# Performance work log

Measured on AMD Instinct MI355X. Metric: run time of the kernel, lower is better.

Reference implementation:

```python
import jax, jax.numpy as jnp
import numpy as np

KSIZE, STRIDE, H, W = 7, 4, 128, 128
NH = (H - KSIZE) // STRIDE + 1  # 31
L = NH * NH                     # 961 patches


def conv2d(x, w, b=None, stride=1):
    y = jax.lax.conv_general_dilated(x, w, (stride, stride), 'VALID',
                                     dimension_numbers=('NCHW', 'OIHW', 'NCHW'))
    if b is not None:
        y = y + b[None, :, None, None]
    return y


def refpad(x):
    return jnp.pad(x, ((0, 0), (0, 0), (1, 1), (1, 1)), mode='reflect')


def unfold(x, k, s):
    # torch.nn.Unfold equivalent, returned as (B, C, k, k, L)
    B, C, Hh, Ww = x.shape
    nh = (Hh - k) // s + 1
    nw = (Ww - k) // s + 1
    hi = (jnp.arange(nh) * s)[:, None] + jnp.arange(k)  # (nh, k)
    wi = (jnp.arange(nw) * s)[:, None] + jnp.arange(k)  # (nw, k)
    p = x[:, :, hi]            # (B, C, nh, k, W)
    p = p[:, :, :, :, wi]      # (B, C, nh, k, nw, k)
    p = p.transpose(0, 1, 3, 5, 2, 4).reshape(B, C, k, k, nh * nw)
    return p


def fold(patches, Hh, Ww, k, s):
    # patches: (B, nh, nw, C, k, k); overlap-add like torch.nn.functional.fold
    B, nh, nw, C = patches.shape[0], patches.shape[1], patches.shape[2], patches.shape[3]
    hi = (jnp.arange(nh) * s)[:, None] + jnp.arange(k)  # (nh, k)
    wi = (jnp.arange(nw) * s)[:, None] + jnp.arange(k)  # (nw, k)
    H_idx = hi[:, None, :, None]  # (nh, 1, k, 1)
    W_idx = wi[None, :, None, :]  # (1, nw, 1, k)
    vals = patches.transpose(0, 3, 1, 2, 4, 5)  # (B, C, nh, nw, k, k)
    out = jnp.zeros((B, C, Hh, Ww), patches.dtype)
    return out.at[:, :, H_idx, W_idx].add(vals)


def setup_inputs() -> dict:
    key = jax.random.key(0)
    ks = jax.random.split(key, 16)
    Cin, Ci = 32, 16            # in_channels, inter_channels
    F_in = KSIZE * KSIZE * Ci   # 784
    F_out = F_in // 4           # 196
    s = 0.05
    d = {
        'x':       jax.random.normal(ks[0], (8, Cin, H, W), jnp.float32),
        'g_w':     jax.random.normal(ks[1], (Ci, Cin, 3, 3), jnp.float32) * s,
        'g_b':     jax.random.normal(ks[2], (Ci,), jnp.float32) * s,
        'w_w':     jax.random.normal(ks[3], (Ci, Cin, 3, 3), jnp.float32) * s,
        'w_b':     jax.random.normal(ks[4], (Ci,), jnp.float32) * s,
        'theta_w': jax.random.normal(ks[5], (Cin, Ci, 1, 1), jnp.float32) * s,
        'theta_b': jax.random.normal(ks[6], (Cin,), jnp.float32) * s,
        'fc1_w':   jax.random.normal(ks[7], (F_out, F_in), jnp.float32) * s,
        'fc1_b':   jax.random.normal(ks[8], (F_out,), jnp.float32) * s,
        'mconv_w': jax.random.normal(ks[9], (L, L), jnp.float32) * s,
        'mconv_b': jax.random.normal(ks[10], (L,), jnp.float32) * s,
        'mfc_w':   jax.random.normal(ks[11], (L, L), jnp.float32) * s,
        'mfc_b':   jax.random.normal(ks[12], (L,), jnp.float32) * s,
        'c1_w':    jax.random.normal(ks[13], (Cin // 2, Cin, 3, 3), jnp.float32) * s,
        'c2_w':    jax.random.normal(ks[14], (Cin, Cin // 2, 1, 1), jnp.float32) * s,
    }
    return d


def reference(x, g_w, g_b, w_w, w_b, theta_w, theta_b, fc1_w, fc1_b,
              mconv_w, mconv_b, mfc_w, mfc_b, c1_w, c2_w):
    residual = x
    x1 = conv2d(refpad(x), g_w, g_b)        # (B, Ci, H, W)
    x2 = conv2d(refpad(x), w_w, w_b)        # (B, Ci, H, W)
    x3 = conv2d(x1, theta_w, theta_b)       # (B, Cin, H, W)
    B = x.shape[0]
    Cin = x.shape[1]

    p6 = unfold(x1, KSIZE, STRIDE).transpose(0, 4, 1, 2, 3).reshape(B, L, -1)   # (B,L,Ci*49)
    p4 = unfold(x2, KSIZE, STRIDE).transpose(0, 4, 1, 2, 3).reshape(B, L, -1)   # (B,L,Ci*49)
    p62 = unfold(x3, KSIZE, STRIDE).transpose(0, 4, 1, 2, 3).reshape(B, L, -1)  # (B,L,Cin*49)

    wf = p4 @ fc1_w.T + fc1_b   # (B, L, F)
    xf = p6 @ fc1_w.T + fc1_b   # (B, L, F)
    A = jnp.einsum('blf,bmf->blm', wf, xf)  # (B, L, L)

    # Ti1 (Conv1d k=1 over patch dim) + Ti2 (Linear over patch dim, transposed)
    Ti = jnp.einsum('nc,bcm->bnm', mconv_w + mfc_w, A) + (mconv_b + mfc_b)[None, :, None]
    mask = jax.nn.sigmoid(Ti)
    mask_b = (mask != 0.0).astype(A.dtype)

    scale = wf.shape[-1] ** -0.5
    Am = jax.nn.softmax(A * mask * scale, axis=-1) * mask_b  # (B, L, L)

    y = jnp.einsum('blm,bmf->blf', Am, p62)  # (B, L, Cin*49)
    y = y.reshape(B, NH, NH, Cin, KSIZE, KSIZE)
    out = fold(y, H, W, KSIZE, STRIDE)       # (B, Cin, H, W)

    # BasicBlock: conv3x3(reflect) -> lrelu -> conv1x1 -> lrelu
    o = jax.nn.leaky_relu(conv2d(refpad(out), c1_w), 0.2)
    o = jax.nn.leaky_relu(conv2d(o, c2_w), 0.2)
    out = residual + o
    return Am, out
```

## Files before the change

### kernel.cpp

```cpp
#include <hip/hip_runtime.h>
#include <math.h>

namespace {
constexpr int Bn   = 8;
constexpr int CIN  = 32;
constexpr int CI   = 16;
constexpr int Lp   = 961;
constexpr int FIN  = 784;
constexpr int FOUT = 196;
constexpr int F62  = 1568;

constexpr int FCP  = 224;
constexpr long long FCB = 961LL * FCP;
constexpr int KP   = 992;
constexpr long long WFTB = 196LL * KP;
constexpr long long AMBB = 961LL * KP;
constexpr long long PBTB = 1568LL * KP;
constexpr long long AB   = 961LL * 961;
constexpr int YLD  = 964;
constexpr long long YB = 1568LL * YLD;
constexpr int CKP  = 512;
}

typedef __attribute__((ext_vector_type(8))) short short8x;
typedef __attribute__((ext_vector_type(4))) float floatx4;
typedef __attribute__((ext_vector_type(4))) unsigned short ushort4x;

static __device__ __forceinline__ unsigned short f2bf(float x) {
    unsigned int u = __builtin_bit_cast(unsigned int, x);
    u += 0x7fffu + ((u >> 16) & 1u);
    return (unsigned short)(u >> 16);
}
static __device__ __forceinline__ float bf2f(unsigned short h) {
    return __builtin_bit_cast(float, ((unsigned int)h) << 16);
}

__global__ __launch_bounds__(256)
void prep_k(const float* __restrict__ g_w, const float* __restrict__ w_w,
            const float* __restrict__ c1_w,
            unsigned short* __restrict__ cwh, unsigned short* __restrict__ cwl,
            unsigned short* __restrict__ c1h, unsigned short* __restrict__ c1l,
            const float* __restrict__ mconv_w, const float* __restrict__ mfc_w,
            unsigned short* __restrict__ Mwh, unsigned short* __restrict__ Mwl,
            const float* __restrict__ mconv_b, const float* __restrict__ mfc_b,
            float* __restrict__ Mb,
            const float* __restrict__ fc1w,
            unsigned short* __restrict__ Wh, unsigned short* __restrict__ Wl,
            unsigned short* __restrict__ wfTh, unsigned short* __restrict__ wfTl)
{
    int i = blockIdx.x * 256 + threadIdx.x;
    if (i < 16384) {
        int n = i >> 9, k = i & 511;
        int ci = k >> 4, t = k & 15;
        float v = 0.0f;
        if (t < 9) v = (n < 16) ? g_w[n * 288 + ci * 9 + t]
                                : w_w[(n - 16) * 288 + ci * 9 + t];
        unsigned short h = f2bf(v);
        cwh[i] = h; cwl[i] = f2bf(v - bf2f(h));
    } else if (i < 24576) {
        int k2 = i - 16384;
        int n = k2 >> 9, k = k2 & 511;
        int ci = k >> 4, t = k & 15;
        float v = (t < 9) ? c1_w[n * 288 + ci * 9 + t] : 0.0f;
        unsigned short h = f2bf(v);
        c1h[k2] = h; c1l[k2] = f2bf(v - bf2f(h));
    } else if (i < 977888) {
        int k = i - 24576;
        int n = k / KP, c = k - n * KP;
        float v = (c < 961) ? (mconv_w[n * 961 + c] + mfc_w[n * 961 + c]) : 0.0f;
        unsigned short h = f2bf(v);
        Mwh[k] = h; Mwl[k] = f2bf(v - bf2f(h));
    } else if (i < 978849) {
        int k = i - 977888;
        Mb[k] = mconv_b[k] + mfc_b[k];
    } else if (i < 1183649) {
        int k = i - 978849;
        int n = k / 800, kk = k - n * 800;
        float v = (n < 196 && kk < 784) ? fc1w[n * 784 + kk] : 0.0f;
        unsigned short h = f2bf(v);
        Wh[k] = h; Wl[k] = f2bf(v - bf2f(h));
    } else if (i < 1233825) {
        int k = i - 1183649;
        int row = k >> 5, c = k & 31;
        long long pos = (long long)row * KP + 960 + c;
        wfTh[pos] = 0; wfTl[pos] = 0;
    }
}

template<int NOUT, bool BIAS, bool LEAKY>
__global__ __launch_bounds__(256)
void convmfma_k(const float* __restrict__ x,
                const unsigned short* __restrict__ Bh,
                const unsigned short* __restrict__ Bl,
                const float* __restrict__ b1, const float* __restrict__ b2,
                float* __restrict__ o1, float* __restrict__ o2)
{
    __shared__ unsigned short AsH[128 * 32], AsL[128 * 32];
    __shared__ unsigned short BsH[NOUT * 32], BsL[NOUT * 32];

    const int tid = threadIdx.x;
    const int b   = blockIdx.x & 7;
    const int h   = blockIdx.x >> 3;
    const float* xb = x + (size_t)b * CIN * 16384;

    const int m   = tid & 127;
    const int kh2 = tid >> 7;
    int ghr[3], gwc[3];
    #pragma unroll
    for (int r = 0; r < 3; ++r) {
        int gh = h - 1 + r; ghr[r] = (gh < 0) ? 1 : (gh > 127 ? 126 : gh);
        int gw = m - 1 + r; gwc[r] = (gw < 0) ? 1 : (gw > 127 ? 126 : gw);
    }

    const int lane = tid & 63;
    const int wv   = tid >> 6;
    const int wm   = wv * 32;
    const int fr   = lane & 15;
    const int kq   = lane >> 4;
    constexpr int NF = NOUT / 16;

    floatx4 acc[2][NF];
    #pragma unroll
    for (int i = 0; i < 2; ++i)
        #pragma unroll
        for (int j = 0; j < NF; ++j)
            acc[i][j] = (floatx4){0.f, 0.f, 0.f, 0.f};

    float pv[9];
    short8x pbh0, pbh1, pbl0, pbl1;
    const bool bstage = tid < NOUT * 2;
    const int bn  = tid >> 1;
    const int bk  = tid & 1;

    auto loadA = [&](int ks) {
        const float* src = xb + (ks * 2 + kh2) * 16384;
        #pragma unroll
        for (int j = 0; j < 9; ++j)
            pv[j] = src[ghr[j / 3] * 128 + gwc[j % 3]];
    };
    auto loadB = [&](int ks) {
        if (bstage) {
            const unsigned short* sh = Bh + bn * CKP + ks * 32 + bk * 16;
            const unsigned short* sl = Bl + bn * CKP + ks * 32 + bk * 16;
            pbh0 = *(const short8x*)sh;       pbh1 = *(const short8x*)(sh + 8);
            pbl0 = *(const short8x*)sl;       pbl1 = *(const short8x*)(sl + 8);
        }
    };

    loadA(0); loadB(0);
    for (int ks = 0; ks < 16; ++ks) {
        {
            unsigned short hv[16], lv[16];
            #pragma unroll
            for (int j = 0; j < 16; ++j) {
                float v = (j < 9) ? pv[j] : 0.0f;
                unsigned short hh = f2bf(v);
                hv[j] = hh; lv[j] = f2bf(v - bf2f(hh));
            }
            const int swz = (m >> 1) & 3;
            const int o0 = (kh2 * 2) ^ swz, o1o = (kh2 * 2 + 1) ^ swz;
            *(short8x*)&AsH[m * 32 + o0 * 8]  = ((short8x*)hv)[0];
            *(short8x*)&AsH[m * 32 + o1o * 8] = ((short8x*)hv)[1];
            *(short8x*)&AsL[m * 32 + o0 * 8]  = ((short8x*)lv)[0];
            *(short8x*)&AsL[m * 32 + o1o * 8] = ((short8x*)lv)[1];
        }
        if (bstage) {
            const int swz = (bn >> 1) & 3;
            const int o0 = (bk * 2) ^ swz, o1o = (bk * 2 + 1) ^ swz;
            *(short8x*)&BsH[bn * 32 + o0 * 8]  = pbh0;
            *(short8x*)&BsH[bn * 32 + o1o * 8] = pbh1;
            *(short8x*)&BsL[bn * 32 + o0 * 8]  = pbl0;
            *(short8x*)&BsL[bn * 32 + o1o * 8] = pbl1;
        }
        __syncthreads();
        if (ks < 15) { loadA(ks + 1); loadB(ks + 1); }

        short8x bhf[NF], blf[NF];
        #pragma unroll
        for (int j = 0; j < NF; ++j) {
            int nr = j * 16 + fr;
            int off = nr * 32 + ((kq ^ ((nr >> 1) & 3)) * 8);
            bhf[j] = *(const short8x*)&BsH[off];
            blf[j] = *(const short8x*)&BsL[off];
        }
        #pragma unroll
        for (int i = 0; i < 2; ++i) {
            int mr = wm + i * 16 + fr;
            int off = mr * 32 + ((kq ^ ((mr >> 1) & 3)) * 8);
            short8x ah = *(const short8x*)&AsH[off];
            short8x al = *(const short8x*)&AsL[off];
            #pragma unroll
            for (int j = 0; j < NF; ++j) {
                acc[i][j] = __builtin_amdgcn_mfma_f32_16x16x32_bf16(ah, bhf[j], acc[i][j], 0, 0, 0);
                acc[i][j] = __builtin_amdgcn_mfma_f32_16x16x32_bf16(ah, blf[j], acc[i][j], 0, 0, 0);
                acc[i][j] = __builtin_amdgcn_mfma_f32_16x16x32_bf16(al, bhf[j], acc[i][j], 0, 0, 0);
            }
        }
        __syncthreads();
    }

    #pragma unroll
    for (int j = 0; j < NF; ++j) {
        int n = j * 16 + fr;
        float bnv = 0.0f;
        if constexpr (BIAS) bnv = (n < 16) ? b1[n] : b2[n - 16];
        float* dst;
        if constexpr (NOUT == 32) {
            dst = (n < 16) ? (o1 + (((size_t)b * 16 + n) * 128 + h) * 128)
                           : (o2 + (((size_t)b * 16 + (n - 16)) * 128 + h) * 128);
        } else {
            dst = o1 + (((size_t)b * 16 + n) * 128 + h) * 128;
        }
        #pragma unroll
        for (int i = 0; i < 2; ++i) {
            int wb = wm + i * 16 + kq * 4;
            floatx4 ov;
            #pragma unroll
            for (int r = 0; r < 4; ++r) {
                float v = acc[i][j][r] + bnv;
                if constexpr (LEAKY) v = (v >= 0.0f) ? v : 0.2f * v;
                ov[r] = v;
            }
            *(floatx4*)(dst + wb) = ov;
        }
    }
}

template<bool BIAS, bool LEAKY, bool RESID>
__global__ __launch_bounds__(256)
void conv1x1p_k(const float* __restrict__ src, const float* __restrict__ wgt,
                const float* __restrict__ bias, const float* __restrict__ resid,
                float* __restrict__ out)
{
    int idx = blockIdx.x * 256 + threadIdx.x;
    int pix = idx & 16383;
    int b   = idx >> 14;
    const float* sb = src + (size_t)b * CI * 16384 + pix;
    float s[16];
    #pragma unroll
    for (int ci = 0; ci < CI; ++ci) s[ci] = sb[ci * 16384];
    size_t ob = (size_t)b * 32 * 16384 + pix;
    #pragma unroll
    for (int co = 0; co < 32; ++co) {
        const float* wrow = wgt + co * CI;
        float acc = BIAS ? bias[co] : 0.0f;
        #pragma unroll
        for (int ci = 0; ci < CI; ++ci) acc += wrow[ci] * s[ci];
        if constexpr (LEAKY) acc = (acc >= 0.0f) ? acc : 0.2f * acc;
        if constexpr (RESID) acc += resid[ob + (size_t)co * 16384];
        out[ob + (size_t)co * 16384] = acc;
    }
}

template<bool WRT>
__global__ __launch_bounds__(256)
void fcmfma_k(const float* __restrict__ xsrc,
              const unsigned short* __restrict__ Wh,
              const unsigned short* __restrict__ Wl,
              const float* __restrict__ bias,
              unsigned short* __restrict__ Dh, unsigned short* __restrict__ Dl,
              unsigned short* __restrict__ DTh, unsigned short* __restrict__ DTl)
{
    __shared__ unsigned short AsH[64*32], AsL[64*32], BsH[64*32], BsL[64*32];
    const int tid = threadIdx.x;
    const int tm0 = (blockIdx.x >> 2) * 64;
    const int tn0 = (blockIdx.x & 3) * 64;

    const int lr = tid >> 2;
    const int lc = tid & 3;
    const int gm = tm0 + lr;
    const bool mok = gm < 7688;
    int gbase = 0;
    if (mok) {
        int b = gm / 961, pi = gm - b * 961;
        int ih = pi / 31, iw = pi - ih * 31;
        gbase = b * 262144 + ih * 512 + iw * 4;
    }
    const int pc = ((lc ^ ((lr >> 1) & 3))) * 8;
    const unsigned short* Whr = Wh + (tn0 + lr) * 800;
    const unsigned short* Wlr = Wl + (tn0 + lr) * 800;

    const int lane = tid & 63, wv = tid >> 6;
    const int wm = (wv >> 1) * 32, wn = (wv & 1) * 32;
    const int fr = lane & 15, kq = lane >> 4;

    floatx4 acc[2][2];
    #pragma unroll
    for (int i = 0; i < 2; ++i)
        #pragma unroll
        for (int j = 0; j < 2; ++j)
            acc[i][j] = (floatx4){0.f, 0.f, 0.f, 0.f};

    float pv[8];
    short8x pwh, pwl;
    auto loadA = [&](int k0) {
        #pragma unroll
        for (int j = 0; j < 8; ++j) {
            int k = k0 + lc * 8 + j;
            float v = 0.0f;
            if (mok && k < 784) {
                int c  = k / 49, r = k - c * 49;
                int kh = r / 7,  kw = r - kh * 7;
                v = xsrc[gbase + c * 16384 + kh * 128 + kw];
            }
            pv[j] = v;
        }
    };
    auto loadW = [&](int k0) {
        pwh = *(const short8x*)(Whr + k0 + lc * 8);
        pwl = *(const short8x*)(Wlr + k0 + lc * 8);
    };

    loadA(0); loadW(0);
    for (int k0 = 0; k0 < 800; k0 += 32) {
        unsigned short hv[8], lv[8];
        #pragma unroll
        for (int j = 0; j < 8; ++j) {
            unsigned short h = f2bf(pv[j]);
            hv[j] = h; lv[j] = f2bf(pv[j] - bf2f(h));
        }
        *(short8x*)&AsH[lr * 32 + pc] = *(short8x*)hv;
        *(short8x*)&AsL[lr * 32 + pc] = *(short8x*)lv;
        *(short8x*)&BsH[lr * 32 + pc] = pwh;
        *(short8x*)&BsL[lr * 32 + pc] = pwl;
        __syncthreads();
        if (k0 + 32 < 800) { loadA(k0 + 32); loadW(k0 + 32); }
        short8x ah[2], al[2], bh[2], bl[2];
        #pragma unroll
        for (int i = 0; i < 2; ++i) {
            int mr = wm + i * 16 + fr;
            int off = mr * 32 + ((kq ^ ((mr >> 1) & 3)) * 8);
            ah[i] = *(const short8x*)&AsH[off];
            al[i] = *(const short8x*)&AsL[off];
        }
        #pragma unroll
        for (int j = 0; j < 2; ++j) {
            int nr = wn + j * 16 + fr;
            int off = nr * 32 + ((kq ^ ((nr >> 1) & 3)) * 8);
            bh[j] = *(const short8x*)&BsH[off];
            bl[j] = *(const short8x*)&BsL[off];
        }
        #pragma unroll
        for (int i = 0; i < 2; ++i)
            #pragma unroll
            for (int j = 0; j < 2; ++j) {
                acc[i][j] = __builtin_amdgcn_mfma_f32_16x16x32_bf16(ah[i], bh[j], acc[i][j], 0, 0, 0);
                acc[i][j] = __builtin_amdgcn_mfma_f32_16x16x32_bf16(ah[i], bl[j], acc[i][j], 0, 0, 0);
                acc[i][j] = __builtin_amdgcn_mfma_f32_16x16x32_bf16(al[i], bh[j], acc[i][j], 0, 0, 0);
            }
        __syncthreads();
    }

    #pragma unroll
    for (int j = 0; j < 2; ++j) {
        int n = tn0 + wn + j * 16 + fr;
        if (n >= FCP) continue;
        float bn = (n < 196) ? bias[n] : 0.0f;
        #pragma unroll
        for (int i = 0; i < 2; ++i) {
            #pragma unroll
            for (int r = 0; r < 4; ++r) {
                int l = tm0 + wm + i * 16 + kq * 4 + r;
                if (l >= 7688) continue;
                int b = l / 961, pi = l - b * 961;
                float v = (n < 196) ? (acc[i][j][r] + bn) : 0.0f;
                unsigned short h = f2bf(v);
                unsigned short lo = f2bf(v - bf2f(h));
                long long base = (long long)b * FCB + (long long)pi * FCP + n;
                Dh[base] = h;
                Dl[base] = lo;
                if constexpr (WRT) {
                    if (n < 196) {
                        long long tb = (long long)b * WFTB + (long long)n * KP + pi;
                        DTh[tb] = h;
                        DTl[tb] = lo;
                    }
                }
            }
        }
    }
}

__global__ __launch_bounds__(256)
void w2mfma_k(const unsigned short* __restrict__ Xhi,
              const unsigned short* __restrict__ Xlo,
              const unsigned short* __restrict__ Yhi,
              const unsigned short* __restrict__ Ylo,
              unsigned short* __restrict__ W2h,
              unsigned short* __restrict__ W2l)
{
    __shared__ unsigned short XsH[4096], XsL[4096], YsH[4096], YsL[4096];
    const int b   = blockIdx.x & 7;
    const int t   = blockIdx.x >> 3;
    const int tm0 = (t >> 1) * 128;
    const int tn0 = (t & 1) * 128;
    const unsigned short* Ybh = Yhi + (long long)b * WFTB;
    const unsigned short* Ybl = Ylo + (long long)b * WFTB;
    const int tid = threadIdx.x;

    const int sr  = tid >> 1;
    const int sc0 = (tid & 1) * 2;
    const bool xok = (tm0 + sr) < 961;
    const bool yok = (tn0 + sr) < 196;
    const unsigned short* Xrh = Xhi + (long long)(tm0 + sr) * KP;
    const unsigned short* Xrl = Xlo + (long long)(tm0 + sr) * KP;
    const unsigned short* Yrh = Ybh + (long long)(tn0 + sr) * KP;
    const unsigned short* Yrl = Ybl + (long long)(tn0 + sr) * KP;
    const int swz = (sr >> 1) & 3;

    const int lane = tid & 63;
    const int wv   = tid >> 6;
    const int wm   = (wv >> 1) * 64, wn = (wv & 1) * 64;
    const int fr   = lane & 15;
    const int kq   = lane >> 4;

    floatx4 acc[4][4];
    #pragma unroll
    for (int i = 0; i < 4; ++i)
        #pragma unroll
        for (int j = 0; j < 4; ++j)
            acc[i][j] = (floatx4){0.f, 0.f, 0.f, 0.f};

    const short8x zz = {0,0,0,0,0,0,0,0};
    short8x pxh[2], pxl[2], pyh[2], pyl[2];
    auto loadK = [&](int k0) {
        #pragma unroll
        for (int c = 0; c < 2; ++c) {
            int kc = sc0 + c;
            pxh[c] = xok ? *(const short8x*)(Xrh + k0 + kc * 8) : zz;
            pxl[c] = xok ? *(const short8x*)(Xrl + k0 + kc * 8) : zz;
            pyh[c] = yok ? *(const short8x*)(Yrh + k0 + kc * 8) : zz;
            pyl[c] = yok ? *(const short8x*)(Yrl + k0 + kc * 8) : zz;
        }
    };

    loadK(0);
    for (int k0 = 0; k0 < KP; k0 += 32) {
        #pragma unroll
        for (int c = 0; c < 2; ++c) {
            int pc = (sc0 + c) ^ swz;
            *(short8x*)&XsH[sr * 32 + pc * 8] = pxh[c];
            *(short8x*)&XsL[sr * 32 + pc * 8] = pxl[c];
            *(short8x*)&YsH[sr * 32 + pc * 8] = pyh[c];
            *(short8x*)&YsL[sr * 32 + pc * 8] = pyl[c];
        }
        __syncthreads();
        if (k0 + 32 < KP) loadK(k0 + 32);
        short8x bh[4], bl[4];
        #pragma unroll
        for (int j = 0; j < 4; ++j) {
            int nr = wn + j * 16 + fr;
            int off = nr * 32 + ((kq ^ ((nr >> 1) & 3)) * 8);
            bh[j] = *(const short8x*)&YsH[off];
            bl[j] = *(const short8x*)&YsL[off];
        }
        #pragma unroll
        for (int i = 0; i < 4; ++i) {
            int mr = wm + i * 16 + fr;
            int off = mr * 32 + ((kq ^ ((mr >> 1) & 3)) * 8);
            short8x ah = *(const short8x*)&XsH[off];
            short8x al = *(const short8x*)&XsL[off];
            #pragma unroll
            for (int j = 0; j < 4; ++j) {
                acc[i][j] = __builtin_amdgcn_mfma_f32_16x16x32_bf16(ah, bh[j], acc[i][j], 0, 0, 0);
                acc[i][j] = __builtin_amdgcn_mfma_f32_16x16x32_bf16(ah, bl[j], acc[i][j], 0, 0, 0);
                acc[i][j] = __builtin_amdgcn_mfma_f32_16x16x32_bf16(al, bh[j], acc[i][j], 0, 0, 0);
            }
        }
        __syncthreads();
    }

    unsigned short* Wh2 = W2h + (long long)b * FCB;
    unsigned short* Wl2 = W2l + (long long)b * FCB;
    #pragma unroll
    for (int j = 0; j < 4; ++j) {
        int f = tn0 + wn + j * 16 + fr;
        if (f >= FCP) continue;
        #pragma unroll
        for (int i = 0; i < 4; ++i) {
            int lb = tm0 + wm + i * 16 + kq * 4;
            #pragma unroll
            for (int r = 0; r < 4; ++r) {
                int l = lb + r;
                if (l >= 961) continue;
                float v = acc[i][j][r];
                unsigned short h = f2bf(v);
                long long pos = (long long)l * FCP + f;
                Wh2[pos] = h;
                Wl2[pos] = f2bf(v - bf2f(h));
            }
        }
    }
}

__global__ __launch_bounds__(256, 2)
void atimfma_k(const unsigned short* __restrict__ Wfh,
               const unsigned short* __restrict__ Wfl,
               const unsigned short* __restrict__ W2h,
               const unsigned short* __restrict__ W2l,
               const unsigned short* __restrict__ Xfh,
               const unsigned short* __restrict__ Xfl,
               const float* __restrict__ Mb,
               float* __restrict__ Sout)
{
    const int b   = blockIdx.x & 7;
    const int t   = blockIdx.x >> 3;
    const int tm0 = (t >> 3) * 128;
    const int tn0 = (t & 7) * 128;
    const int tid = threadIdx.x;

    const int lane = tid & 63;
    const int wv   = tid >> 6;
    const int wm   = (wv >> 1) * 64, wn = (wv & 1) * 64;
    const int fr   = lane & 15;
    const int kq   = lane >> 4;

    const long long bb = (long long)b * FCB;
    const unsigned short* A1h = Wfh + bb;
    const unsigned short* A1l = Wfl + bb;
    const unsigned short* A2h = W2h + bb;
    const unsigned short* A2l = W2l + bb;
    const unsigned short* Byh = Xfh + bb;
    const unsigned short* Byl = Xfl + bb;

    int aoff[4], boff[4];
    #pragma unroll
    for (int i = 0; i < 4; ++i) {
        int r = tm0 + wm + i * 16 + fr; if (r > 960) r = 960;
        aoff[i] = r * FCP + kq * 8;
    }
    #pragma unroll
    for (int j = 0; j < 4; ++j) {
        int r = tn0 + wn + j * 16 + fr; if (r > 960) r = 960;
        boff[j] = r * FCP + kq * 8;
    }

    floatx4 accA[4][4], accT[4][4];
    #pragma unroll
    for (int i = 0; i < 4; ++i)
        #pragma unroll
        for (int j = 0; j < 4; ++j) {
            accA[i][j] = (floatx4){0.f, 0.f, 0.f, 0.f};
            accT[i][j] = (floatx4){0.f, 0.f, 0.f, 0.f};
        }

    short8x f1h[2][4], f1l[2][4], f2h[2][4], f2l[2][4], fbh[2][4], fbl[2][4];

    #pragma unroll
    for (int j = 0; j < 4; ++j) {
        fbh[0][j] = *(const short8x*)(Byh + boff[j]);
        fbl[0][j] = *(const short8x*)(Byl + boff[j]);
    }
    #pragma unroll
    for (int i = 0; i < 4; ++i) {
        f1h[0][i] = *(const short8x*)(A1h + aoff[i]);
        f1l[0][i] = *(const short8x*)(A1l + aoff[i]);
        f2h[0][i] = *(const short8x*)(A2h + aoff[i]);
        f2l[0][i] = *(const short8x*)(A2l + aoff[i]);
    }

    #pragma unroll
    for (int ks = 0; ks < 7; ++ks) {
        const int cur = ks & 1, nxt = cur ^ 1;
        if (ks < 6) {
            const int k0 = (ks + 1) * 32;
            #pragma unroll
            for (int j = 0; j < 4; ++j) {
                fbh[nxt][j] = *(const short8x*)(Byh + boff[j] + k0);
                fbl[nxt][j] = *(const short8x*)(Byl + boff[j] + k0);
            }
            #pragma unroll
            for (int i = 0; i < 4; ++i) {
                f1h[nxt][i] = *(const short8x*)(A1h + aoff[i] + k0);
                f1l[nxt][i] = *(const short8x*)(A1l + aoff[i] + k0);
                f2h[nxt][i] = *(const short8x*)(A2h + aoff[i] + k0);
                f2l[nxt][i] = *(const short8x*)(A2l + aoff[i] + k0);
            }
        }
        #pragma unroll
        for (int i = 0; i < 4; ++i) {
            #pragma unroll
            for (int j = 0; j < 4; ++j) {
                accA[i][j] = __builtin_amdgcn_mfma_f32_16x16x32_bf16(f1h[cur][i], fbh[cur][j], accA[i][j], 0, 0, 0);
                accA[i][j] = __builtin_amdgcn_mfma_f32_16x16x32_bf16(f1h[cur][i], fbl[cur][j], accA[i][j], 0, 0, 0);
                accA[i][j] = __builtin_amdgcn_mfma_f32_16x16x32_bf16(f1l[cur][i], fbh[cur][j], accA[i][j], 0, 0, 0);
                accT[i][j] = __builtin_amdgcn_mfma_f32_16x16x32_bf16(f2h[cur][i], fbh[cur][j], accT[i][j], 0, 0, 0);
                accT[i][j] = __builtin_amdgcn_mfma_f32_16x16x32_bf16(f2h[cur][i], fbl[cur][j], accT[i][j], 0, 0, 0);
                accT[i][j] = __builtin_amdgcn_mfma_f32_16x16x32_bf16(f2l[cur][i], fbh[cur][j], accT[i][j], 0, 0, 0);
            }
        }
    }

    const float scale = 0.07142857142857142f;
    float* Sb = Sout + (long long)b * AB;
    #pragma unroll
    for (int j = 0; j < 4; ++j) {
        int m = tn0 + wn + j * 16 + fr;
        if (m >= 961) continue;
        #pragma unroll
        for (int i = 0; i < 4; ++i) {
            int lb = tm0 + wm + i * 16 + kq * 4;
            #pragma unroll
            for (int r = 0; r < 4; ++r) {
                int l = lb + r;
                if (l >= 961) continue;
                float ti = accT[i][j][r] + Mb[l];
                float mask = 1.0f / (1.0f + expf(-ti));
                Sb[(long long)l * 961 + m] = accA[i][j][r] * mask * scale;
            }
        }
    }
}

__global__ __launch_bounds__(256)
void softmax_mask_k(const float* __restrict__ S, float* __restrict__ Am,
                    unsigned short* __restrict__ Amb)
{
    int row = blockIdx.x;
    const float* srow = S + (long long)row * Lp;
    float*       orow = Am + (long long)row * Lp;
    unsigned short* brow = Amb + (long long)row * KP;
    int tid = threadIdx.x;

    float s[4], mb[4];
    float lmax = -INFINITY;
    #pragma unroll
    for (int j = 0; j < 4; ++j) {
        int m = tid + j * 256;
        if (m < Lp) {
            float v = srow[m];
            s[j]  = v;
            mb[j] = (v != 0.0f) ? 1.0f : 0.0f;
            lmax  = fmaxf(lmax, v);
        } else { s[j] = -INFINITY; mb[j] = 0.0f; }
    }
    __shared__ float red[256];
    red[tid] = lmax; __syncthreads();
    #pragma unroll
    for (int off = 128; off > 0; off >>= 1) {
        if (tid < off) red[tid] = fmaxf(red[tid], red[tid + off]);
        __syncthreads();
    }
    float rmax = red[0];
    __syncthreads();

    float e[4];
    float lsum = 0.0f;
    #pragma unroll
    for (int j = 0; j < 4; ++j) {
        int m = tid + j * 256;
        e[j] = (m < Lp) ? expf(s[j] - rmax) : 0.0f;
        lsum += e[j];
    }
    red[tid] = lsum; __syncthreads();
    #pragma unroll
    for (int off = 128; off > 0; off >>= 1) {
        if (tid < off) red[tid] += red[tid + off];
        __syncthreads();
    }
    float inv = 1.0f / red[0];
    #pragma unroll
    for (int j = 0; j < 4; ++j) {
        int m = tid + j * 256;
        if (m < Lp) {
            float v = e[j] * inv * mb[j];
            orow[m] = v;
            brow[m] = f2bf(v);
        } else if (m < KP) {
            brow[m] = 0;
        }
    }
}

__global__ __launch_bounds__(256)
void p62bt_k(const float* __restrict__ x3, unsigned short* __restrict__ out)
{
    int idx = blockIdx.x * 256 + threadIdx.x;
    if (idx >= 8 * 1568 * 124) return;
    int ck = idx % 124;
    int t  = idx / 124;
    int n  = t % 1568;
    int b  = t / 1568;
    int c = n / 49, rr = n - c * 49;
    int kh = rr / 7, kw = rr - kh * 7;
    const float* src = x3 + (long long)b * 524288 + c * 16384 + kh * 128 + kw;
    int k = ck * 8;
    unsigned short v[8];
    #pragma unroll
    for (int j = 0; j < 8; ++j) {
        int kk = k + j;
        if (kk < Lp) {
            int ih = kk / 31, iw = kk - ih * 31;
            v[j] = f2bf(src[ih * 512 + iw * 4]);
        } else v[j] = 0;
    }
    *(short8x*)(out + ((long long)b * 1568 + n) * KP + k) = *(short8x*)v;
}

__global__ __launch_bounds__(256)
void ymfma_k(const unsigned short* __restrict__ Amb,
             const unsigned short* __restrict__ Pbt,
             unsigned short* __restrict__ yT)
{
    __shared__ unsigned short As[128 * 32];
    __shared__ unsigned short Bs[128 * 32];
    const int b   = blockIdx.x & 7;
    const int t   = blockIdx.x >> 3;
    const int tn0 = (t % 13) * 128;
    const int tm0 = (t / 13) * 128;
    const unsigned short* Ab = Amb + (long long)b * AMBB;
    const unsigned short* Bb = Pbt + (long long)b * PBTB;
    const int tid = threadIdx.x;

    const int sr  = tid >> 1;
    const int sc0 = (tid & 1) * 2;
    const bool aok = (tm0 + sr) < Lp;
    const bool bok = (tn0 + sr) < F62;
    const unsigned short* Arow = Ab + (long long)(tm0 + sr) * KP;
    const unsigned short* Brow = Bb + (long long)(tn0 + sr) * KP;
    const int swz = (sr >> 1) & 3;

    const int lane = tid & 63;
    const int wv   = tid >> 6;
    const int wm   = (wv >> 1) * 64, wn = (wv & 1) * 64;
    const int fr   = lane & 15;
    const int kq   = lane >> 4;

    floatx4 acc[4][4];
    #pragma unroll
    for (int i = 0; i < 4; ++i)
        #pragma unroll
        for (int j = 0; j < 4; ++j)
            acc[i][j] = (floatx4){0.f, 0.f, 0.f, 0.f};

    const short8x zz = {0,0,0,0,0,0,0,0};
    short8x pa[2], pb[2];
    auto loadK = [&](int k0) {
        #pragma unroll
        for (int c = 0; c < 2; ++c) {
            int kc = sc0 + c;
            pa[c] = aok ? *(const short8x*)(Arow + k0 + kc * 8) : zz;
            pb[c] = bok ? *(const short8x*)(Brow + k0 + kc * 8) : zz;
        }
    };

    loadK(0);
    for (int k0 = 0; k0 < Lp; k0 += 32) {
        #pragma unroll
        for (int c = 0; c < 2; ++c) {
            int pc = (sc0 + c) ^ swz;
            *(short8x*)&As[sr * 32 + pc * 8] = pa[c];
            *(short8x*)&Bs[sr * 32 + pc * 8] = pb[c];
        }
        __syncthreads();
        if (k0 + 32 < Lp) loadK(k0 + 32);
        short8x af[4], bfr[4];
        #pragma unroll
        for (int i = 0; i < 4; ++i) {
            int mr = wm + i * 16 + fr;
            af[i] = *(const short8x*)&As[mr * 32 + ((kq ^ ((mr >> 1) & 3)) * 8)];
        }
        #pragma unroll
        for (int j = 0; j < 4; ++j) {
            int nr = wn + j * 16 + fr;
            bfr[j] = *(const short8x*)&Bs[nr * 32 + ((kq ^ ((nr >> 1) & 3)) * 8)];
        }
        #pragma unroll
        for (int i = 0; i < 4; ++i)
            #pragma unroll
            for (int j = 0; j < 4; ++j)
                acc[i][j] = __builtin_amdgcn_mfma_f32_16x16x32_bf16(
                                af[i], bfr[j], acc[i][j], 0, 0, 0);
        __syncthreads();
    }

    unsigned short* Yb = yT + (long long)b * YB;
    #pragma unroll
    for (int j = 0; j < 4; ++j) {
        int n = tn0 + wn + j * 16 + fr;
        if (n >= F62) continue;
        unsigned short* Yr = Yb + (long long)n * YLD;
        #pragma unroll
        for (int i = 0; i < 4; ++i) {
            int lb = tm0 + wm + i * 16 + kq * 4;
            if (lb >= Lp) continue;
            ushort4x hv;
            #pragma unroll
            for (int r = 0; r < 4; ++r) hv[r] = f2bf(acc[i][j][r]);
            if (lb + 3 < Lp) {
                *(ushort4x*)(Yr + lb) = hv;
            } else {
                #pragma unroll
                for (int r = 0; r < 4; ++r)
                    if (lb + r < Lp) Yr[lb + r] = hv[r];
            }
        }
    }
}

__global__ __launch_bounds__(256)
void foldg_k(const unsigned short* __restrict__ yT, float* __restrict__ out)
{
    int idx = blockIdx.x * 256 + threadIdx.x;
    int wc = idx & 127;
    int hr = (idx >> 7) & 127;
    int c  = (idx >> 14) & 31;
    int b  = idx >> 19;
    int ih_lo = (hr >= 6) ? ((hr - 3) >> 2) : 0;
    int ih_hi = min(hr >> 2, 30);
    int iw_lo = (wc >= 6) ? ((wc - 3) >> 2) : 0;
    int iw_hi = min(wc >> 2, 30);
    const unsigned short* Yb = yT + (long long)b * YB + (long long)c * 49 * YLD;
    float acc = 0.0f;
    for (int ih = ih_lo; ih <= ih_hi; ++ih) {
        int kh = hr - 4 * ih;
        for (int iw = iw_lo; iw <= iw_hi; ++iw) {
            int kw = wc - 4 * iw;
            acc += bf2f(Yb[(kh * 7 + kw) * YLD + ih * 31 + iw]);
        }
    }
    out[idx] = acc;
}

extern "C" void kernel_launch(void* const* d_in, const int* in_sizes, int n_in,
                              void* d_out, int out_size, void* d_ws, size_t ws_size,
                              hipStream_t stream)
{
    const float* x       = (const float*)d_in[0];
    const float* g_w     = (const float*)d_in[1];
    const float* g_b     = (const float*)d_in[2];
    const float* w_w     = (const float*)d_in[3];
    const float* w_b     = (const float*)d_in[4];
    const float* theta_w = (const float*)d_in[5];
    const float* theta_b = (const float*)d_in[6];
    const float* fc1_w   = (const float*)d_in[7];
    const float* fc1_b   = (const float*)d_in[8];
    const float* mconv_w = (const float*)d_in[9];
    const float* mconv_b = (const float*)d_in[10];
    const float* mfc_w   = (const float*)d_in[11];
    const float* mfc_b   = (const float*)d_in[12];
    const float* c1_w    = (const float*)d_in[13];
    const float* c2_w    = (const float*)d_in[14];

    float* Am_out    = (float*)d_out;
    float* final_out = Am_out + (size_t)Bn * Lp * Lp;

    float* ws = (float*)d_ws;
    float* x1    = ws;
    float* x2    = ws + 2097152;
    float* x3    = ws + 4194304;
    unsigned short* xf_hi = (unsigned short*)(ws + 8388608);
    unsigned short* xf_lo = (unsigned short*)(ws + 9249664);
    unsigned short* wf_hi = (unsigned short*)(ws + 10110720);
    unsigned short* wf_lo = (unsigned short*)(ws + 10971776);
    float* Abuf  = ws + 11832832;
    unsigned short* wfT_hi = (unsigned short*)(ws + 19221000);
    unsigned short* wfT_lo = (unsigned short*)(ws + 19998728);
    unsigned short* W2_hi  = (unsigned short*)(ws + 20776456);
    unsigned short* W2_lo  = (unsigned short*)(ws + 21637512);
    unsigned short* Mw_hi = (unsigned short*)(ws + 26847496);
    unsigned short* Mw_lo = (unsigned short*)(ws + 27324152);
    float* Mb    = ws + 27800808;
    unsigned short* fc1wh = (unsigned short*)(ws + 27801832);
    unsigned short* fc1wl = (unsigned short*)(ws + 27904232);
    unsigned short* cwh = (unsigned short*)(ws + 4194304);
    unsigned short* cwl = cwh + 16384;
    unsigned short* c1h = (unsigned short*)(ws + 28006632);
    unsigned short* c1l = c1h + 8192;
    unsigned short* Am_bf16 = (unsigned short*)x1;
    unsigned short* p62bT   = (unsigned short*)Abuf;
    unsigned short* yT      = wfT_hi;

    prep_k<<<4821, 256, 0, stream>>>(
        g_w, w_w, c1_w, cwh, cwl, c1h, c1l,
        mconv_w, mfc_w, Mw_hi, Mw_lo,
        mconv_b, mfc_b, Mb, fc1_w, fc1wh, fc1wl,
        wfT_hi, wfT_lo);

    convmfma_k<32, true, false><<<1024, 256, 0, stream>>>(
        x, cwh, cwl, g_b, w_b, x1, x2);

    conv1x1p_k<true, false, false><<<512, 256, 0, stream>>>(
        x1, theta_w, theta_b, nullptr, x3);

    fcmfma_k<false><<<484, 256, 0, stream>>>(
        x1, fc1wh, fc1wl, fc1_b, xf_hi, xf_lo, nullptr, nullptr);
    fcmfma_k<true><<<484, 256, 0, stream>>>(
        x2, fc1wh, fc1wl, fc1_b, wf_hi, wf_lo, wfT_hi, wfT_lo);

    w2mfma_k<<<128, 256, 0, stream>>>(
        Mw_hi, Mw_lo, wfT_hi, wfT_lo, W2_hi, W2_lo);

    atimfma_k<<<512, 256, 0, stream>>>(
        wf_hi, wf_lo, W2_hi, W2_lo, xf_hi, xf_lo, Mb, Abuf);

    softmax_mask_k<<<7688, 256, 0, stream>>>(Abuf, Am_out, Am_bf16);

    p62bt_k<<<6077, 256, 0, stream>>>(x3, p62bT);

    ymfma_k<<<832, 256, 0, stream>>>(Am_bf16, p62bT, yT);

    foldg_k<<<16384, 256, 0, stream>>>(yT, x3);

    convmfma_k<16, false, true><<<1024, 256, 0, stream>>>(
        x3, c1h, c1l, nullptr, nullptr, x1, nullptr);

    conv1x1p_k<false, true, true><<<512, 256, 0, stream>>>(
        x1, c2_w, nullptr, x, final_out);
}
```

Baseline: 476.6 us.

## Load MFMA fragments directly from global memory in ymfma_k, dropping LDS staging

Reworks the Am·P GEMM kernel so each wave loads its bf16 MFMA operand fragments straight from global memory into registers, double-buffered across a fully unrolled 31-step K loop. This removes the shared-memory tiles and both __syncthreads per K step. Out-of-range rows are clamped instead of zero-filled, and the kernel now asks for 2 blocks per CU. The trade-off is that data shared across waves is fetched redundantly from global memory or L2 instead of being reused through LDS. Register pressure also rises from the unrolled double buffers.

```diff
diff --git a/kernel.cpp b/kernel.cpp
--- a/kernel.cpp
+++ b/kernel.cpp
@@ -697,13 +697,11 @@
     *(short8x*)(out + ((long long)b * 1568 + n) * KP + k) = *(short8x*)v;
 }
 
-__global__ __launch_bounds__(256)
+__global__ __launch_bounds__(256, 2)
 void ymfma_k(const unsigned short* __restrict__ Amb,
              const unsigned short* __restrict__ Pbt,
              unsigned short* __restrict__ yT)
 {
-    __shared__ unsigned short As[128 * 32];
-    __shared__ unsigned short Bs[128 * 32];
     const int b   = blockIdx.x & 7;
     const int t   = blockIdx.x >> 3;
     const int tn0 = (t % 13) * 128;
@@ -712,20 +710,24 @@
     const unsigned short* Bb = Pbt + (long long)b * PBTB;
     const int tid = threadIdx.x;
 
-    const int sr  = tid >> 1;
-    const int sc0 = (tid & 1) * 2;
-    const bool aok = (tm0 + sr) < Lp;
-    const bool bok = (tn0 + sr) < F62;
-    const unsigned short* Arow = Ab + (long long)(tm0 + sr) * KP;
-    const unsigned short* Brow = Bb + (long long)(tn0 + sr) * KP;
-    const int swz = (sr >> 1) & 3;
-
     const int lane = tid & 63;
     const int wv   = tid >> 6;
     const int wm   = (wv >> 1) * 64, wn = (wv & 1) * 64;
     const int fr   = lane & 15;
     const int kq   = lane >> 4;
 
+    int aoff[4], boff[4];
+    #pragma unroll
+    for (int i = 0; i < 4; ++i) {
+        int r = tm0 + wm + i * 16 + fr; if (r > 960) r = 960;
+        aoff[i] = r * KP + kq * 8;
+    }
+    #pragma unroll
+    for (int j = 0; j < 4; ++j) {
+        int r = tn0 + wn + j * 16 + fr; if (r > 1567) r = 1567;
+        boff[j] = r * KP + kq * 8;
+    }
+
     floatx4 acc[4][4];
     #pragma unroll
     for (int i = 0; i < 4; ++i)
@@ -733,45 +735,30 @@
         for (int j = 0; j < 4; ++j)
             acc[i][j] = (floatx4){0.f, 0.f, 0.f, 0.f};
 
-    const short8x zz = {0,0,0,0,0,0,0,0};
-    short8x pa[2], pb[2];
-    auto loadK = [&](int k0) {
-        #pragma unroll
-        for (int c = 0; c < 2; ++c) {
-            int kc = sc0 + c;
-            pa[c] = aok ? *(const short8x*)(Arow + k0 + kc * 8) : zz;
-            pb[c] = bok ? *(const short8x*)(Brow + k0 + kc * 8) : zz;
-        }
-    };
-
-    loadK(0);
-    for (int k0 = 0; k0 < Lp; k0 += 32) {
-        #pragma unroll
-        for (int c = 0; c < 2; ++c) {
-            int pc = (sc0 + c) ^ swz;
-            *(short8x*)&As[sr * 32 + pc * 8] = pa[c];
-            *(short8x*)&Bs[sr * 32 + pc * 8] = pb[c];
-        }
-        __syncthreads();
-        if (k0 + 32 < Lp) loadK(k0 + 32);
-        short8x af[4], bfr[4];
-        #pragma unroll
-        for (int i = 0; i < 4; ++i) {
-            int mr = wm + i * 16 + fr;
-            af[i] = *(const short8x*)&As[mr * 32 + ((kq ^ ((mr >> 1) & 3)) * 8)];
-        }
-        #pragma unroll
-        for (int j = 0; j < 4; ++j) {
-            int nr = wn + j * 16 + fr;
-            bfr[j] = *(const short8x*)&Bs[nr * 32 + ((kq ^ ((nr >> 1) & 3)) * 8)];
+    short8x fa[2][4], fb[2][4];
+    #pragma unroll
+    for (int i = 0; i < 4; ++i) fa[0][i] = *(const short8x*)(Ab + aoff[i]);
+    #pragma unroll
+    for (int j = 0; j < 4; ++j) fb[0][j] = *(const short8x*)(Bb + boff[j]);
+
+    #pragma unroll
+    for (int ks = 0; ks < 31; ++ks) {
+        const int cur = ks & 1, nxt = cur ^ 1;
+        if (ks < 30) {
+            const int k0 = (ks + 1) * 32;
+            #pragma unroll
+            for (int i = 0; i < 4; ++i)
+                fa[nxt][i] = *(const short8x*)(Ab + aoff[i] + k0);
+            #pragma unroll
+            for (int j = 0; j < 4; ++j)
+                fb[nxt][j] = *(const short8x*)(Bb + boff[j] + k0);
         }
         #pragma unroll
         for (int i = 0; i < 4; ++i)
             #pragma unroll
             for (int j = 0; j < 4; ++j)
                 acc[i][j] = __builtin_amdgcn_mfma_f32_16x16x32_bf16(
-                                af[i], bfr[j], acc[i][j], 0, 0, 0);
-        __syncthreads();
+                                fa[cur][i], fb[cur][j], acc[i][j], 0, 0, 0);
     }
 
     unsigned short* Yb = yT + (long long)b * YB;
```

Result: slower. 496.5 us (+4.2%).

## Convert conv inputs to channels-last bf16 split and merge FC launches

Applied to the files above, without the earlier changes.

Adds a pre-pass that transposes the NCHW fp32 input into channels-last hi/lo bf16 pairs. The 3x3 conv kernel then stages three padded rows once in shared memory and loops over the 9 taps with K=32 channels, instead of im2col-ing 16 K-steps padded from 9 to 16 with per-step conversion and syncs. Conv weights are repacked to a dense 288-wide tap-major layout and read straight from global memory. The two fc GEMM launches are also merged into one grid. The change adds two extra transpose kernels and their global traffic, and reuses the workspace region for the channels-last buffers.

```diff
diff --git a/kernel.cpp b/kernel.cpp
--- a/kernel.cpp
+++ b/kernel.cpp
@@ -19,7 +19,7 @@
 constexpr long long AB   = 961LL * 961;
 constexpr int YLD  = 964;
 constexpr long long YB = 1568LL * YLD;
-constexpr int CKP  = 512;
+constexpr int CK   = 288;
 }
 
 typedef __attribute__((ext_vector_type(8))) short short8x;
@@ -49,68 +49,98 @@
             unsigned short* __restrict__ wfTh, unsigned short* __restrict__ wfTl)
 {
     int i = blockIdx.x * 256 + threadIdx.x;
-    if (i < 16384) {
-        int n = i >> 9, k = i & 511;
-        int ci = k >> 4, t = k & 15;
-        float v = 0.0f;
-        if (t < 9) v = (n < 16) ? g_w[n * 288 + ci * 9 + t]
-                                : w_w[(n - 16) * 288 + ci * 9 + t];
+    if (i < 9216) {
+        int n = i / CK, k = i - n * CK;
+        int t = k >> 5, ci = k & 31;
+        float v = (n < 16) ? g_w[n * 288 + ci * 9 + t]
+                           : w_w[(n - 16) * 288 + ci * 9 + t];
         unsigned short h = f2bf(v);
         cwh[i] = h; cwl[i] = f2bf(v - bf2f(h));
-    } else if (i < 24576) {
-        int k2 = i - 16384;
-        int n = k2 >> 9, k = k2 & 511;
-        int ci = k >> 4, t = k & 15;
-        float v = (t < 9) ? c1_w[n * 288 + ci * 9 + t] : 0.0f;
+    } else if (i < 13824) {
+        int k2 = i - 9216;
+        int n = k2 / CK, k = k2 - n * CK;
+        int t = k >> 5, ci = k & 31;
+        float v = c1_w[n * 288 + ci * 9 + t];
         unsigned short h = f2bf(v);
         c1h[k2] = h; c1l[k2] = f2bf(v - bf2f(h));
-    } else if (i < 977888) {
-        int k = i - 24576;
+    } else if (i < 967136) {
+        int k = i - 13824;
         int n = k / KP, c = k - n * KP;
         float v = (c < 961) ? (mconv_w[n * 961 + c] + mfc_w[n * 961 + c]) : 0.0f;
         unsigned short h = f2bf(v);
         Mwh[k] = h; Mwl[k] = f2bf(v - bf2f(h));
-    } else if (i < 978849) {
-        int k = i - 977888;
+    } else if (i < 968097) {
+        int k = i - 967136;
         Mb[k] = mconv_b[k] + mfc_b[k];
-    } else if (i < 1183649) {
-        int k = i - 978849;
+    } else if (i < 1172897) {
+        int k = i - 968097;
         int n = k / 800, kk = k - n * 800;
         float v = (n < 196 && kk < 784) ? fc1w[n * 784 + kk] : 0.0f;
         unsigned short h = f2bf(v);
         Wh[k] = h; Wl[k] = f2bf(v - bf2f(h));
-    } else if (i < 1233825) {
-        int k = i - 1183649;
+    } else if (i < 1223073) {
+        int k = i - 1172897;
         int row = k >> 5, c = k & 31;
         long long pos = (long long)row * KP + 960 + c;
         wfTh[pos] = 0; wfTl[pos] = 0;
     }
 }
 
+__global__ __launch_bounds__(256)
+void cls_k(const float* __restrict__ src,
+           unsigned short* __restrict__ dh_, unsigned short* __restrict__ dl_)
+{
+    __shared__ float T[4096];
+    const int b = blockIdx.x & 7, h = blockIdx.x >> 3;
+    const float* sb = src + (size_t)b * 32 * 16384 + h * 128;
+    for (int i = threadIdx.x; i < 4096; i += 256) {
+        int ci = i >> 7, w = i & 127;
+        T[i] = sb[ci * 16384 + w];
+    }
+    __syncthreads();
+    long long obase = ((long long)b * 16384 + (long long)h * 128) * 32;
+    for (int i = threadIdx.x; i < 512; i += 256) {
+        int w = i >> 2, o = i & 3;
+        unsigned short hv[8], lv[8];
+        #pragma unroll
+        for (int e = 0; e < 8; ++e) {
+            float v = T[(o * 8 + e) * 128 + w];
+            unsigned short hh = f2bf(v);
+            hv[e] = hh; lv[e] = f2bf(v - bf2f(hh));
+        }
+        *(short8x*)(dh_ + obase + w * 32 + o * 8) = *(short8x*)hv;
+        *(short8x*)(dl_ + obase + w * 32 + o * 8) = *(short8x*)lv;
+    }
+}
+
 template<int NOUT, bool BIAS, bool LEAKY>
 __global__ __launch_bounds__(256)
-void convmfma_k(const float* __restrict__ x,
-                const unsigned short* __restrict__ Bh,
-                const unsigned short* __restrict__ Bl,
-                const float* __restrict__ b1, const float* __restrict__ b2,
-                float* __restrict__ o1, float* __restrict__ o2)
-{
-    __shared__ unsigned short AsH[128 * 32], AsL[128 * 32];
-    __shared__ unsigned short BsH[NOUT * 32], BsL[NOUT * 32];
+void convcl_k(const unsigned short* __restrict__ Ih,
+              const unsigned short* __restrict__ Il,
+              const unsigned short* __restrict__ Bh,
+              const unsigned short* __restrict__ Bl,
+              const float* __restrict__ b1, const float* __restrict__ b2,
+              float* __restrict__ o1, float* __restrict__ o2)
+{
+    __shared__ unsigned short IsH[12480];
+    __shared__ unsigned short IsL[12480];
 
     const int tid = threadIdx.x;
     const int b   = blockIdx.x & 7;
     const int h   = blockIdx.x >> 3;
-    const float* xb = x + (size_t)b * CIN * 16384;
-
-    const int m   = tid & 127;
-    const int kh2 = tid >> 7;
-    int ghr[3], gwc[3];
-    #pragma unroll
-    for (int r = 0; r < 3; ++r) {
-        int gh = h - 1 + r; ghr[r] = (gh < 0) ? 1 : (gh > 127 ? 126 : gh);
-        int gw = m - 1 + r; gwc[r] = (gw < 0) ? 1 : (gw > 127 ? 126 : gw);
-    }
+
+    for (int i = tid; i < 1560; i += 256) {
+        int p = i >> 2, o = i & 3;
+        int dh = (p >= 260) ? 2 : (p >= 130) ? 1 : 0;
+        int c  = p - dh * 130;
+        int gh = h - 1 + dh; gh = (gh < 0) ? 1 : (gh > 127 ? 126 : gh);
+        int gw = c - 1;      gw = (gw < 0) ? 1 : (gw > 127 ? 126 : gw);
+        long long src = (((long long)b * 16384 + gh * 128 + gw) << 5) + o * 8;
+        int dst = p * 32 + ((o ^ ((c >> 1) & 3)) << 3);
+        *(short8x*)&IsH[dst] = *(const short8x*)(Ih + src);
+        *(short8x*)&IsL[dst] = *(const short8x*)(Il + src);
+    }
+    __syncthreads();
 
     const int lane = tid & 63;
     const int wv   = tid >> 6;
@@ -126,77 +156,29 @@
         for (int j = 0; j < NF; ++j)
             acc[i][j] = (floatx4){0.f, 0.f, 0.f, 0.f};
 
-    float pv[9];
-    short8x pbh0, pbh1, pbl0, pbl1;
-    const bool bstage = tid < NOUT * 2;
-    const int bn  = tid >> 1;
-    const int bk  = tid & 1;
-
-    auto loadA = [&](int ks) {
-        const float* src = xb + (ks * 2 + kh2) * 16384;
-        #pragma unroll
-        for (int j = 0; j < 9; ++j)
-            pv[j] = src[ghr[j / 3] * 128 + gwc[j % 3]];
-    };
-    auto loadB = [&](int ks) {
-        if (bstage) {
-            const unsigned short* sh = Bh + bn * CKP + ks * 32 + bk * 16;
-            const unsigned short* sl = Bl + bn * CKP + ks * 32 + bk * 16;
-            pbh0 = *(const short8x*)sh;       pbh1 = *(const short8x*)(sh + 8);
-            pbl0 = *(const short8x*)sl;       pbl1 = *(const short8x*)(sl + 8);
-        }
-    };
-
-    loadA(0); loadB(0);
-    for (int ks = 0; ks < 16; ++ks) {
-        {
-            unsigned short hv[16], lv[16];
-            #pragma unroll
-            for (int j = 0; j < 16; ++j) {
-                float v = (j < 9) ? pv[j] : 0.0f;
-                unsigned short hh = f2bf(v);
-                hv[j] = hh; lv[j] = f2bf(v - bf2f(hh));
-            }
-            const int swz = (m >> 1) & 3;
-            const int o0 = (kh2 * 2) ^ swz, o1o = (kh2 * 2 + 1) ^ swz;
-            *(short8x*)&AsH[m * 32 + o0 * 8]  = ((short8x*)hv)[0];
-            *(short8x*)&AsH[m * 32 + o1o * 8] = ((short8x*)hv)[1];
-            *(short8x*)&AsL[m * 32 + o0 * 8]  = ((short8x*)lv)[0];
-            *(short8x*)&AsL[m * 32 + o1o * 8] = ((short8x*)lv)[1];
-        }
-        if (bstage) {
-            const int swz = (bn >> 1) & 3;
-            const int o0 = (bk * 2) ^ swz, o1o = (bk * 2 + 1) ^ swz;
-            *(short8x*)&BsH[bn * 32 + o0 * 8]  = pbh0;
-            *(short8x*)&BsH[bn * 32 + o1o * 8] = pbh1;
-            *(short8x*)&BsL[bn * 32 + o0 * 8]  = pbl0;
-            *(short8x*)&BsL[bn * 32 + o1o * 8] = pbl1;
-        }
-        __syncthreads();
-        if (ks < 15) { loadA(ks + 1); loadB(ks + 1); }
-
-        short8x bhf[NF], blf[NF];
+    #pragma unroll
+    for (int t = 0; t < 9; ++t) {
+        const int dh = t / 3, dw = t % 3;
+        short8x bh_[NF], bl_[NF];
         #pragma unroll
         for (int j = 0; j < NF; ++j) {
             int nr = j * 16 + fr;
-            int off = nr * 32 + ((kq ^ ((nr >> 1) & 3)) * 8);
-            bhf[j] = *(const short8x*)&BsH[off];
-            blf[j] = *(const short8x*)&BsL[off];
+            bh_[j] = *(const short8x*)(Bh + nr * CK + t * 32 + kq * 8);
+            bl_[j] = *(const short8x*)(Bl + nr * CK + t * 32 + kq * 8);
         }
         #pragma unroll
         for (int i = 0; i < 2; ++i) {
-            int mr = wm + i * 16 + fr;
-            int off = mr * 32 + ((kq ^ ((mr >> 1) & 3)) * 8);
-            short8x ah = *(const short8x*)&AsH[off];
-            short8x al = *(const short8x*)&AsL[off];
+            int col = wm + i * 16 + fr + dw;
+            int off = (dh * 130 + col) * 32 + ((kq ^ ((col >> 1) & 3)) << 3);
+            short8x ah = *(const short8x*)&IsH[off];
+            short8x al = *(const short8x*)&IsL[off];
             #pragma unroll
             for (int j = 0; j < NF; ++j) {
-                acc[i][j] = __builtin_amdgcn_mfma_f32_16x16x32_bf16(ah, bhf[j], acc[i][j], 0, 0, 0);
-                acc[i][j] = __builtin_amdgcn_mfma_f32_16x16x32_bf16(ah, blf[j], acc[i][j], 0, 0, 0);
-                acc[i][j] = __builtin_amdgcn_mfma_f32_16x16x32_bf16(al, bhf[j], acc[i][j], 0, 0, 0);
-            }
-        }
-        __syncthreads();
+                acc[i][j] = __builtin_amdgcn_mfma_f32_16x16x32_bf16(ah, bh_[j], acc[i][j], 0, 0, 0);
+                acc[i][j] = __builtin_amdgcn_mfma_f32_16x16x32_bf16(ah, bl_[j], acc[i][j], 0, 0, 0);
+                acc[i][j] = __builtin_amdgcn_mfma_f32_16x16x32_bf16(al, bh_[j], acc[i][j], 0, 0, 0);
+            }
+        }
     }
 
     #pragma unroll
@@ -252,19 +234,24 @@
     }
 }
 
-template<bool WRT>
 __global__ __launch_bounds__(256)
-void fcmfma_k(const float* __restrict__ xsrc,
-              const unsigned short* __restrict__ Wh,
-              const unsigned short* __restrict__ Wl,
-              const float* __restrict__ bias,
-              unsigned short* __restrict__ Dh, unsigned short* __restrict__ Dl,
-              unsigned short* __restrict__ DTh, unsigned short* __restrict__ DTl)
+void fcmfma2_k(const float* __restrict__ x1s, const float* __restrict__ x2s,
+               const unsigned short* __restrict__ Wh,
+               const unsigned short* __restrict__ Wl,
+               const float* __restrict__ bias,
+               unsigned short* __restrict__ Xfh, unsigned short* __restrict__ Xfl,
+               unsigned short* __restrict__ Wfh, unsigned short* __restrict__ Wfl,
+               unsigned short* __restrict__ DTh, unsigned short* __restrict__ DTl)
 {
     __shared__ unsigned short AsH[64*32], AsL[64*32], BsH[64*32], BsL[64*32];
     const int tid = threadIdx.x;
-    const int tm0 = (blockIdx.x >> 2) * 64;
-    const int tn0 = (blockIdx.x & 3) * 64;
+    const bool wrt = blockIdx.x >= 484;
+    const int bid = wrt ? (int)blockIdx.x - 484 : (int)blockIdx.x;
+    const float* xsrc = wrt ? x2s : x1s;
+    unsigned short* Dh = wrt ? Wfh : Xfh;
+    unsigned short* Dl = wrt ? Wfl : Xfl;
+    const int tm0 = (bid >> 2) * 64;
+    const int tn0 = (bid & 3) * 64;
 
     const int lr = tid >> 2;
     const int lc = tid & 3;
@@ -369,12 +356,10 @@
                 long long base = (long long)b * FCB + (long long)pi * FCP + n;
                 Dh[base] = h;
                 Dl[base] = lo;
-                if constexpr (WRT) {
-                    if (n < 196) {
-                        long long tb = (long long)b * WFTB + (long long)n * KP + pi;
-                        DTh[tb] = h;
-                        DTl[tb] = lo;
-                    }
+                if (wrt && n < 196) {
+                    long long tb = (long long)b * WFTB + (long long)n * KP + pi;
+                    DTh[tb] = h;
+                    DTl[tb] = lo;
                 }
             }
         }
@@ -867,26 +852,31 @@
     unsigned short* cwl = cwh + 16384;
     unsigned short* c1h = (unsigned short*)(ws + 28006632);
     unsigned short* c1l = c1h + 8192;
+    unsigned short* xclH = (unsigned short*)(ws + 11832832);
+    unsigned short* xclL = (unsigned short*)(ws + 13929984);
     unsigned short* Am_bf16 = (unsigned short*)x1;
     unsigned short* p62bT   = (unsigned short*)Abuf;
     unsigned short* yT      = wfT_hi;
-
-    prep_k<<<4821, 256, 0, stream>>>(
+    unsigned short* fclH    = xclH;
+    unsigned short* fclL    = xclL;
+
+    prep_k<<<4778, 256, 0, stream>>>(
         g_w, w_w, c1_w, cwh, cwl, c1h, c1l,
         mconv_w, mfc_w, Mw_hi, Mw_lo,
         mconv_b, mfc_b, Mb, fc1_w, fc1wh, fc1wl,
         wfT_hi, wfT_lo);
 
-    convmfma_k<32, true, false><<<1024, 256, 0, stream>>>(
-        x, cwh, cwl, g_b, w_b, x1, x2);
+    cls_k<<<1024, 256, 0, stream>>>(x, xclH, xclL);
+
+    convcl_k<32, true, false><<<1024, 256, 0, stream>>>(
+        xclH, xclL, cwh, cwl, g_b, w_b, x1, x2);
 
     conv1x1p_k<true, false, false><<<512, 256, 0, stream>>>(
         x1, theta_w, theta_b, nullptr, x3);
 
-    fcmfma_k<false><<<484, 256, 0, stream>>>(
-        x1, fc1wh, fc1wl, fc1_b, xf_hi, xf_lo, nullptr, nullptr);
-    fcmfma_k<true><<<484, 256, 0, stream>>>(
-        x2, fc1wh, fc1wl, fc1_b, wf_hi, wf_lo, wfT_hi, wfT_lo);
+    fcmfma2_k<<<968, 256, 0, stream>>>(
+        x1, x2, fc1wh, fc1wl, fc1_b,
+        xf_hi, xf_lo, wf_hi, wf_lo, wfT_hi, wfT_lo);
 
     w2mfma_k<<<128, 256, 0, stream>>>(
         Mw_hi, Mw_lo, wfT_hi, wfT_lo, W2_hi, W2_lo);
@@ -902,8 +892,10 @@
 
     foldg_k<<<16384, 256, 0, stream>>>(yT, x3);
 
-    convmfma_k<16, false, true><<<1024, 256, 0, stream>>>(
-        x3, c1h, c1l, nullptr, nullptr, x1, nullptr);
+    cls_k<<<1024, 256, 0, stream>>>(x3, fclH, fclL);
+
+    convcl_k<16, false, true><<<1024, 256, 0, stream>>>(
+        fclH, fclL, c1h, c1l, nullptr, nullptr, x1, nullptr);
 
     conv1x1p_k<false, true, true><<<512, 256, 0, stream>>>(
         x1, c2_w, nullptr, x, final_out);
```

Result: no change. 474.1 us (-0.5%).
